# Performance work log

Hardware: AMD Instinct MI355X
Metric: run time of the kernel (lower is better)

## Reference

```python
import jax, jax.numpy as jnp
import numpy as np

H, B, D, C = 6, 512, 2048, 1000   # heads (5 ICs + backbone exit), batch, feat dim, classes
TAU = 0.5                          # confidence_threshold


def setup_inputs() -> dict:
    key = jax.random.key(0)
    k1, k2, k3, k4 = jax.random.split(key, 4)
    feats = jax.random.normal(k1, (H, B, D), dtype=jnp.float32)          # pooled reps at each exit
    W = jax.random.normal(k2, (H, D, C), dtype=jnp.float32) * 0.07       # per-head classifier weights
    b = jax.random.normal(k3, (H, C), dtype=jnp.float32) * 0.1
    y_true = jax.random.randint(k4, (B,), 0, C)
    return {"feats": feats, "W": W, "b": b, "y_true": y_true}


def reference(feats, W, b, y_true):
    # Per-head logits for every sample (vectorized replacement for the shrinking-batch loop).
    logits = jnp.einsum('hbd,hdc->hbc', feats, W) + b[:, None, :]        # [H, B, C]
    logp = jax.nn.log_softmax(logits, axis=-1)
    conf = jnp.exp(logp).max(axis=-1)                                    # [H, B] max softmax prob (prob_conf=True)

    # Early-exit routing: first head with conf >= TAU; else head with max confidence
    # (argmax returns the first occurrence, matching the strict '>' update in find_exit).
    exited = conf >= TAU                                                  # [H, B]
    any_exit = exited.any(axis=0)                                         # [B]
    first_exit = jnp.argmax(exited, axis=0)                               # [B] first True along heads
    best_conf = jnp.argmax(conf, axis=0)                                  # [B] fallback exit
    exit_idx = jnp.where(any_exit, first_exit, best_conf)                 # [B] == sample_exited_at

    # Gather the chosen head's logits per sample (vectorized masked-scatter of sample_outputs).
    outputs = jnp.take_along_axis(logits, exit_idx[None, :, None], axis=0)[0]   # [B, C]

    # criterion_ic: cross-entropy loss + accuracy on routed outputs
    out_logp = jax.nn.log_softmax(outputs, axis=-1)
    loss = -jnp.take_along_axis(out_logp, y_true[:, None], axis=1).mean()
    acc = (outputs.argmax(axis=-1) == y_true).astype(jnp.float32).mean()
    return outputs, exit_idx.astype(jnp.int32), loss, acc
```

## Files before the change

### kernel.cpp

```cpp
#include <hip/hip_runtime.h>
#include <hip/hip_bf16.h>
#include <math.h>

#define Hn 6
#define Bn 512
#define Dn 2048
#define Cn 1000
#define Cpad 1024
#define TAUv 0.5f
#define KSPLIT 4
#define KPER (Dn / KSPLIT)
#define NIT (KPER / 32)

typedef unsigned int u32;
typedef unsigned short u16;
typedef __attribute__((ext_vector_type(8))) short short8;
typedef __attribute__((ext_vector_type(4))) float f32x4;

union FragU { u32 d[4]; short8 s; };

__device__ __forceinline__ u32 cvt_pk2(float f0, float f1) {
  union { __hip_bfloat162 h; u32 u; } cv;
  cv.h = __float22bfloat162_rn(make_float2(f0, f1));
  return cv.u;
}

__device__ __forceinline__ void pack8f(const float* f, FragU& hi, FragU& lo) {
  float r[8];
#pragma unroll
  for (int i = 0; i < 4; ++i) {
    const u32 d = cvt_pk2(f[2 * i], f[2 * i + 1]);
    hi.d[i] = d;
    r[2 * i]     = f[2 * i]     - __uint_as_float(d << 16);
    r[2 * i + 1] = f[2 * i + 1] - __uint_as_float(d & 0xffff0000u);
  }
#pragma unroll
  for (int i = 0; i < 4; ++i) lo.d[i] = cvt_pk2(r[2 * i], r[2 * i + 1]);
}

__device__ __forceinline__ void dma16(const void* g, void* l) {
  __builtin_amdgcn_global_load_lds(
      (const __attribute__((address_space(1))) u32*)g,
      (__attribute__((address_space(3))) u32*)l, 16, 0, 0);
}

__global__ __launch_bounds__(256, 2) void gemm_k(
    const float* __restrict__ feats, const float* __restrict__ W,
    const float* __restrict__ bias, float* __restrict__ logits)
{
  const int h  = blockIdx.z >> 2;
  const int kz = blockIdx.z & 3;
  const int m0 = blockIdx.y * 128;
  const int n0 = blockIdx.x * 128;
  const int t = threadIdx.x, lane = t & 63, w = t >> 6;

  __shared__ __align__(16) float lds[2][8192];

  const int rA = (w & 1) * 64 + (lane >> 3);
  const int qA = (lane & 7) ^ ((lane >> 3) & 7);
  const float* gsrcA = feats + ((size_t)(h * Bn + m0 + rA)) * Dn + kz * KPER + qA * 4;
  const size_t gciA = (size_t)8 * Dn;
  const int dstA = w * 8192 + lane * 16;
  const int kb = (w - 2) * 16 + (lane >> 5);
  const int pB = lane & 31;
  const float* Wrow = W + ((size_t)h * Dn + kz * KPER) * Cn;
  const int dstB = 16384 + (w - 2) * 8192 + lane * 16;

  const int fl = lane & 15, fq = lane >> 4;
  const int wm = (w & 1) * 64, wn = (w >> 1) * 64;
  const int sxor = fl & 7;

  f32x4 acc[4][4];
#pragma unroll
  for (int i = 0; i < 4; ++i)
#pragma unroll
    for (int j = 0; j < 4; ++j) acc[i][j] = (f32x4){0.f, 0.f, 0.f, 0.f};

#define STAGE(TILE)                                                                   \
  {                                                                                   \
    char* sb = (char*)&lds[(TILE) & 1][0];                                            \
    if (w < 2) {                                                                      \
      const float* g = gsrcA + (size_t)(TILE) * 32;                                   \
      _Pragma("unroll")                                                               \
      for (int i = 0; i < 8; ++i) dma16(g + i * gciA, sb + dstA + i * 1024);          \
    } else {                                                                          \
      const size_t kt0 = (size_t)(TILE) * 32;                                         \
      _Pragma("unroll")                                                               \
      for (int i = 0; i < 8; ++i) {                                                   \
        const int kl = kb + 2 * i;                                                    \
        const int pc = pB ^ (((kl >> 3) & 3) << 2);                                   \
        int col = n0 + pc * 4;                                                        \
        col = (col + 3 < Cn) ? col : (Cn - 4);                                        \
        dma16(Wrow + (kt0 + kl) * Cn + col, sb + dstB + i * 1024);                    \
      }                                                                               \
    }                                                                                 \
  }

#define COMPUTE_TILE(IT)                                                              \
  {                                                                                   \
    const char*  ab = (const char*)&lds[(IT) & 1][0];                                 \
    const float* bb = (const float*)(ab + 16384);                                     \
    FragU ah[4], al[4];                                                               \
    _Pragma("unroll")                                                                 \
    for (int mt = 0; mt < 4; ++mt) {                                                  \
      const int r = wm + mt * 16 + fl;                                                \
      const float4 v0 = *(const float4*)(ab + r * 128 + ((((fq * 2)    ) ^ sxor) * 16)); \
      const float4 v1 = *(const float4*)(ab + r * 128 + ((((fq * 2) + 1) ^ sxor) * 16)); \
      float f[8] = {v0.x, v0.y, v0.z, v0.w, v1.x, v1.y, v1.z, v1.w};                  \
      pack8f(f, ah[mt], al[mt]);                                                      \
    }                                                                                 \
    _Pragma("unroll")                                                                 \
    for (int nt = 0; nt < 4; ++nt) {                                                  \
      const int n = wn + nt * 16 + fl;                                                \
      const int nsw = ((((n >> 2) ^ (fq << 2)) << 2) | (n & 3));                      \
      float f[8];                                                                     \
      _Pragma("unroll")                                                               \
      for (int e = 0; e < 8; ++e) f[e] = bb[(fq * 8 + e) * 128 + nsw];                \
      FragU bh, bl;                                                                   \
      pack8f(f, bh, bl);                                                              \
      _Pragma("unroll")                                                               \
      for (int mt = 0; mt < 4; ++mt) {                                                \
        acc[mt][nt] = __builtin_amdgcn_mfma_f32_16x16x32_bf16(ah[mt].s, bh.s, acc[mt][nt], 0, 0, 0); \
        acc[mt][nt] = __builtin_amdgcn_mfma_f32_16x16x32_bf16(ah[mt].s, bl.s, acc[mt][nt], 0, 0, 0); \
        acc[mt][nt] = __builtin_amdgcn_mfma_f32_16x16x32_bf16(al[mt].s, bh.s, acc[mt][nt], 0, 0, 0); \
      }                                                                               \
    }                                                                                 \
  }

  STAGE(0);

  for (int it = 0; it < NIT - 1; ++it) {
    STAGE(it + 1);
    asm volatile("s_waitcnt vmcnt(8)" ::: "memory");
    __builtin_amdgcn_s_barrier();
    __builtin_amdgcn_sched_barrier(0);
    COMPUTE_TILE(it);
    __builtin_amdgcn_sched_barrier(0);
    asm volatile("s_waitcnt lgkmcnt(0)" ::: "memory");
    __builtin_amdgcn_s_barrier();
  }
  asm volatile("s_waitcnt vmcnt(0)" ::: "memory");
  __builtin_amdgcn_s_barrier();
  __builtin_amdgcn_sched_barrier(0);
  COMPUTE_TILE(NIT - 1);
#undef COMPUTE_TILE
#undef STAGE

  float* part = logits + (size_t)kz * ((size_t)Hn * Bn * Cn);
#pragma unroll
  for (int nt = 0; nt < 4; ++nt) {
    const int col = n0 + wn + nt * 16 + fl;
    if (col >= Cn) continue;
    const float bv = (kz == 0) ? bias[(size_t)h * Cn + col] : 0.f;
#pragma unroll
    for (int mt = 0; mt < 4; ++mt) {
      const int rbase = m0 + wm + mt * 16 + fq * 4;
#pragma unroll
      for (int r = 0; r < 4; ++r)
        part[((size_t)h * Bn + rbase + r) * Cn + col] = acc[mt][nt][r] + bv;
    }
  }
}

__global__ __launch_bounds__(256) void confpick_k(
    const float* __restrict__ logits, const int* __restrict__ y,
    float* __restrict__ out, float* __restrict__ out_exit,
    float* __restrict__ loss_b, float* __restrict__ corr_b)
{
  const int b = blockIdx.x, tid = threadIdx.x;
  const int lane = tid & 63, w = tid >> 6;
  const size_t S = (size_t)Hn * Bn * Cn;
  __shared__ float ms[Hn], ss[Hn];

  for (int h = w; h < Hn; h += 4) {
    const float* p = logits + ((size_t)h * Bn + b) * Cn;
    float vv[16];
#pragma unroll
    for (int i = 0; i < 4; ++i) {
      const int c4 = i * 256 + lane * 4;
      if (c4 + 3 < Cn) {
        const float4 v0 = *(const float4*)(p + c4);
        const float4 v1 = *(const float4*)(p + S + c4);
        const float4 v2 = *(const float4*)(p + 2 * S + c4);
        const float4 v3 = *(const float4*)(p + 3 * S + c4);
        vv[4 * i + 0] = v0.x + v1.x + v2.x + v3.x;
        vv[4 * i + 1] = v0.y + v1.y + v2.y + v3.y;
        vv[4 * i + 2] = v0.z + v1.z + v2.z + v3.z;
        vv[4 * i + 3] = v0.w + v1.w + v2.w + v3.w;
      } else {
#pragma unroll
        for (int j = 0; j < 4; ++j) {
          const int c = c4 + j;
          vv[4 * i + j] = (c < Cn) ? p[c] + p[S + c] + p[2 * S + c] + p[3 * S + c]
                                   : -3.4e38f;
        }
      }
    }
    float m = -3.4e38f;
#pragma unroll
    for (int i = 0; i < 16; ++i) m = fmaxf(m, vv[i]);
#pragma unroll
    for (int off = 32; off >= 1; off >>= 1) m = fmaxf(m, __shfl_xor(m, off));
    float s = 0.f;
#pragma unroll
    for (int i = 0; i < 16; ++i) s += (vv[i] > -3.0e38f) ? expf(vv[i] - m) : 0.f;
#pragma unroll
    for (int off = 32; off >= 1; off >>= 1) s += __shfl_xor(s, off);
    if (lane == 0) { ms[h] = m; ss[h] = s; }
  }
  __syncthreads();

  int first = -1, best = 0;
  float bestc = -3.4e38f;
#pragma unroll
  for (int h = 0; h < Hn; ++h) {
    const float c = 1.0f / ss[h];
    if (first < 0 && c >= TAUv) first = h;
    if (c > bestc) { bestc = c; best = h; }
  }
  const int ex = (first >= 0) ? first : best;
  const float* p = logits + ((size_t)ex * Bn + b) * Cn;

  const int c4 = tid * 4;
  float vv[4] = {-3.4e38f, -3.4e38f, -3.4e38f, -3.4e38f};
  if (c4 + 3 < Cn) {
    const float4 v0 = *(const float4*)(p + c4);
    const float4 v1 = *(const float4*)(p + S + c4);
    const float4 v2 = *(const float4*)(p + 2 * S + c4);
    const float4 v3 = *(const float4*)(p + 3 * S + c4);
    vv[0] = v0.x + v1.x + v2.x + v3.x;
    vv[1] = v0.y + v1.y + v2.y + v3.y;
    vv[2] = v0.z + v1.z + v2.z + v3.z;
    vv[3] = v0.w + v1.w + v2.w + v3.w;
  }
  float vm = -3.4e38f; int im = 1 << 30;
#pragma unroll
  for (int j = 0; j < 4; ++j) {
    const int c = c4 + j;
    if (c < Cn) {
      out[(size_t)b * Cn + c] = vv[j];
      if (vv[j] > vm) { vm = vv[j]; im = c; }
    }
  }
#pragma unroll
  for (int off = 32; off >= 1; off >>= 1) {
    const float ov = __shfl_xor(vm, off);
    const int   oi = __shfl_xor(im, off);
    if (ov > vm || (ov == vm && oi < im)) { vm = ov; im = oi; }
  }
  __shared__ float rm[4]; __shared__ int ri[4];
  if (lane == 0) { rm[w] = vm; ri[w] = im; }
  __syncthreads();
  if (tid == 0) {
    float bm = rm[0]; int bi = ri[0];
    for (int q = 1; q < 4; ++q)
      if (rm[q] > bm || (rm[q] == bm && ri[q] < bi)) { bm = rm[q]; bi = ri[q]; }
    const int yt = y[b];
    const float ryt = p[yt] + p[S + yt] + p[2 * S + yt] + p[3 * S + yt];
    const float lp = ryt - ms[ex] - logf(ss[ex]);
    out_exit[b] = (float)ex;
    loss_b[b] = -lp;
    corr_b[b] = (bi == yt) ? 1.f : 0.f;
  }
}

__global__ __launch_bounds__(256) void reduce_k(
    const float* __restrict__ loss_b, const float* __restrict__ corr_b,
    float* __restrict__ scalars)
{
  const int t = threadIdx.x, lane = t & 63, w = t >> 6;
  float l = loss_b[t] + loss_b[t + 256];
  float c = corr_b[t] + corr_b[t + 256];
#pragma unroll
  for (int off = 32; off >= 1; off >>= 1) {
    l += __shfl_xor(l, off);
    c += __shfl_xor(c, off);
  }
  __shared__ float sl[4], sc[4];
  if (lane == 0) { sl[w] = l; sc[w] = c; }
  __syncthreads();
  if (t == 0) {
    scalars[0] = (sl[0] + sl[1] + sl[2] + sl[3]) * (1.0f / (float)Bn);
    scalars[1] = (sc[0] + sc[1] + sc[2] + sc[3]) * (1.0f / (float)Bn);
  }
}

extern "C" void kernel_launch(void* const* d_in, const int* in_sizes, int n_in,
                              void* d_out, int out_size, void* d_ws, size_t ws_size,
                              hipStream_t stream) {
  const float* feats = (const float*)d_in[0];
  const float* W     = (const float*)d_in[1];
  const float* bias  = (const float*)d_in[2];
  const int*   y     = (const int*)d_in[3];
  float* out = (float*)d_out;

  float* logits = (float*)d_ws;
  float* loss_b = logits + (size_t)KSPLIT * Hn * Bn * Cn;
  float* corr_b = loss_b + Bn;
  float* out_exit    = out + (size_t)Bn * Cn;
  float* out_scalars = out + (size_t)Bn * Cn + Bn;

  gemm_k<<<dim3(Cpad / 128, Bn / 128, Hn * KSPLIT), 256, 0, stream>>>(
      feats, W, bias, logits);
  confpick_k<<<Bn, 256, 0, stream>>>(logits, y, out, out_exit, loss_b, corr_b);
  reduce_k<<<1, 256, 0, stream>>>(loss_b, corr_b, out_scalars);
}
```

Baseline: 179.1 us.

## Halve split-K and narrow GEMM N-tile to 64 with three blocks per CU

Changes split-K from 4 to 2 and the N tile from 128 to 64. The grid keeps the same block count while each block does twice the K work with a smaller LDS footprint, and launch bounds now request 3 blocks per CU. The B-tile staging, swizzle and per-wave wait counts are rewritten for the narrower tile, and the confpick kernel sums only 2 partial slabs. This cuts partial-sum write and read traffic, at the cost of less A reuse per block, longer serial K loops and a possible register-pressure squeeze.

Result: no change. 181.7 us (+1.4%).

```diff
diff --git a/kernel.cpp b/kernel.cpp
--- a/kernel.cpp
+++ b/kernel.cpp
@@ -8,7 +8,7 @@
 #define Cn 1000
 #define Cpad 1024
 #define TAUv 0.5f
-#define KSPLIT 4
+#define KSPLIT 2
 #define KPER (Dn / KSPLIT)
 #define NIT (KPER / 32)
 
@@ -44,37 +44,38 @@
       (__attribute__((address_space(3))) u32*)l, 16, 0, 0);
 }
 
-__global__ __launch_bounds__(256, 2) void gemm_k(
+__global__ __launch_bounds__(256, 3) void gemm_k(
     const float* __restrict__ feats, const float* __restrict__ W,
     const float* __restrict__ bias, float* __restrict__ logits)
 {
-  const int h  = blockIdx.z >> 2;
-  const int kz = blockIdx.z & 3;
+  const int h  = blockIdx.z >> 1;
+  const int kz = blockIdx.z & 1;
   const int m0 = blockIdx.y * 128;
-  const int n0 = blockIdx.x * 128;
+  const int n0 = blockIdx.x * 64;
   const int t = threadIdx.x, lane = t & 63, w = t >> 6;
 
-  __shared__ __align__(16) float lds[2][8192];
+  __shared__ __align__(16) float lds[2][6144];
 
   const int rA = (w & 1) * 64 + (lane >> 3);
   const int qA = (lane & 7) ^ ((lane >> 3) & 7);
   const float* gsrcA = feats + ((size_t)(h * Bn + m0 + rA)) * Dn + kz * KPER + qA * 4;
   const size_t gciA = (size_t)8 * Dn;
   const int dstA = w * 8192 + lane * 16;
-  const int kb = (w - 2) * 16 + (lane >> 5);
-  const int pB = lane & 31;
+
+  const int kb = (w - 2) * 16 + (lane >> 4);
+  const int cB = lane & 15;
   const float* Wrow = W + ((size_t)h * Dn + kz * KPER) * Cn;
-  const int dstB = 16384 + (w - 2) * 8192 + lane * 16;
+  const int dstB = 16384 + (w - 2) * 4096 + lane * 16;
 
   const int fl = lane & 15, fq = lane >> 4;
-  const int wm = (w & 1) * 64, wn = (w >> 1) * 64;
+  const int wm = (w & 1) * 64, wn = (w >> 1) * 32;
   const int sxor = fl & 7;
 
-  f32x4 acc[4][4];
+  f32x4 acc[4][2];
 #pragma unroll
   for (int i = 0; i < 4; ++i)
 #pragma unroll
-    for (int j = 0; j < 4; ++j) acc[i][j] = (f32x4){0.f, 0.f, 0.f, 0.f};
+    for (int j = 0; j < 2; ++j) acc[i][j] = (f32x4){0.f, 0.f, 0.f, 0.f};
 
 #define STAGE(TILE)                                                                   \
   {                                                                                   \
@@ -86,14 +87,20 @@
     } else {                                                                          \
       const size_t kt0 = (size_t)(TILE) * 32;                                         \
       _Pragma("unroll")                                                               \
-      for (int i = 0; i < 8; ++i) {                                                   \
-        const int kl = kb + 2 * i;                                                    \
-        const int pc = pB ^ (((kl >> 3) & 3) << 2);                                   \
+      for (int i = 0; i < 4; ++i) {                                                   \
+        const int kl = kb + 4 * i;                                                    \
+        const int pc = cB ^ (((kl >> 3) & 1) << 2);                                   \
         int col = n0 + pc * 4;                                                        \
         col = (col + 3 < Cn) ? col : (Cn - 4);                                        \
         dma16(Wrow + (kt0 + kl) * Cn + col, sb + dstB + i * 1024);                    \
       }                                                                               \
     }                                                                                 \
+  }
+
+#define WAITCUR()                                                                     \
+  {                                                                                   \
+    if (w < 2) asm volatile("s_waitcnt vmcnt(8)" ::: "memory");                       \
+    else       asm volatile("s_waitcnt vmcnt(4)" ::: "memory");                       \
   }
 
 #define COMPUTE_TILE(IT)                                                              \
@@ -110,12 +117,12 @@
       pack8f(f, ah[mt], al[mt]);                                                      \
     }                                                                                 \
     _Pragma("unroll")                                                                 \
-    for (int nt = 0; nt < 4; ++nt) {                                                  \
+    for (int nt = 0; nt < 2; ++nt) {                                                  \
       const int n = wn + nt * 16 + fl;                                                \
-      const int nsw = ((((n >> 2) ^ (fq << 2)) << 2) | (n & 3));                      \
+      const int nsw = ((((n >> 2) ^ ((fq & 1) << 2)) << 2) | (n & 3));                \
       float f[8];                                                                     \
       _Pragma("unroll")                                                               \
-      for (int e = 0; e < 8; ++e) f[e] = bb[(fq * 8 + e) * 128 + nsw];                \
+      for (int e = 0; e < 8; ++e) f[e] = bb[(fq * 8 + e) * 64 + nsw];                 \
       FragU bh, bl;                                                                   \
       pack8f(f, bh, bl);                                                              \
       _Pragma("unroll")                                                               \
@@ -131,7 +138,7 @@
 
   for (int it = 0; it < NIT - 1; ++it) {
     STAGE(it + 1);
-    asm volatile("s_waitcnt vmcnt(8)" ::: "memory");
+    WAITCUR();
     __builtin_amdgcn_s_barrier();
     __builtin_amdgcn_sched_barrier(0);
     COMPUTE_TILE(it);
@@ -144,11 +151,12 @@
   __builtin_amdgcn_sched_barrier(0);
   COMPUTE_TILE(NIT - 1);
 #undef COMPUTE_TILE
+#undef WAITCUR
 #undef STAGE
 
   float* part = logits + (size_t)kz * ((size_t)Hn * Bn * Cn);
 #pragma unroll
-  for (int nt = 0; nt < 4; ++nt) {
+  for (int nt = 0; nt < 2; ++nt) {
     const int col = n0 + wn + nt * 16 + fl;
     if (col >= Cn) continue;
     const float bv = (kz == 0) ? bias[(size_t)h * Cn + col] : 0.f;
@@ -181,18 +189,15 @@
       if (c4 + 3 < Cn) {
         const float4 v0 = *(const float4*)(p + c4);
         const float4 v1 = *(const float4*)(p + S + c4);
-        const float4 v2 = *(const float4*)(p + 2 * S + c4);
-        const float4 v3 = *(const float4*)(p + 3 * S + c4);
-        vv[4 * i + 0] = v0.x + v1.x + v2.x + v3.x;
-        vv[4 * i + 1] = v0.y + v1.y + v2.y + v3.y;
-        vv[4 * i + 2] = v0.z + v1.z + v2.z + v3.z;
-        vv[4 * i + 3] = v0.w + v1.w + v2.w + v3.w;
+        vv[4 * i + 0] = v0.x + v1.x;
+        vv[4 * i + 1] = v0.y + v1.y;
+        vv[4 * i + 2] = v0.z + v1.z;
+        vv[4 * i + 3] = v0.w + v1.w;
       } else {
 #pragma unroll
         for (int j = 0; j < 4; ++j) {
           const int c = c4 + j;
-          vv[4 * i + j] = (c < Cn) ? p[c] + p[S + c] + p[2 * S + c] + p[3 * S + c]
-                                   : -3.4e38f;
+          vv[4 * i + j] = (c < Cn) ? p[c] + p[S + c] : -3.4e38f;
         }
       }
     }
@@ -226,12 +231,10 @@
   if (c4 + 3 < Cn) {
     const float4 v0 = *(const float4*)(p + c4);
     const float4 v1 = *(const float4*)(p + S + c4);
-    const float4 v2 = *(const float4*)(p + 2 * S + c4);
-    const float4 v3 = *(const float4*)(p + 3 * S + c4);
-    vv[0] = v0.x + v1.x + v2.x + v3.x;
-    vv[1] = v0.y + v1.y + v2.y + v3.y;
-    vv[2] = v0.z + v1.z + v2.z + v3.z;
-    vv[3] = v0.w + v1.w + v2.w + v3.w;
+    vv[0] = v0.x + v1.x;
+    vv[1] = v0.y + v1.y;
+    vv[2] = v0.z + v1.z;
+    vv[3] = v0.w + v1.w;
   }
   float vm = -3.4e38f; int im = 1 << 30;
 #pragma unroll
@@ -256,7 +259,7 @@
     for (int q = 1; q < 4; ++q)
       if (rm[q] > bm || (rm[q] == bm && ri[q] < bi)) { bm = rm[q]; bi = ri[q]; }
     const int yt = y[b];
-    const float ryt = p[yt] + p[S + yt] + p[2 * S + yt] + p[3 * S + yt];
+    const float ryt = p[yt] + p[S + yt];
     const float lp = ryt - ms[ex] - logf(ss[ex]);
     out_exit[b] = (float)ex;
     loss_b[b] = -lp;
@@ -300,7 +303,7 @@
   float* out_exit    = out + (size_t)Bn * Cn;
   float* out_scalars = out + (size_t)Bn * Cn + Bn;
 
-  gemm_k<<<dim3(Cpad / 128, Bn / 128, Hn * KSPLIT), 256, 0, stream>>>(
+  gemm_k<<<dim3(Cpad / 64, Bn / 128, Hn * KSPLIT), 256, 0, stream>>>(
       feats, W, bias, logits);
   confpick_k<<<Bn, 256, 0, stream>>>(logits, y, out, out_exit, loss_b, corr_b);
   reduce_k<<<1, 256, 0, stream>>>(loss_b, corr_b, out_scalars);
```
